# Optimization experiments

Hardware: AMD Instinct MI355X
Metric: run time of the kernel (lower is better)

## Reference

```python
import jax, jax.numpy as jnp
import numpy as np

D_MODEL = 1024
N_HEADS = 16
HEAD_DIM = D_MODEL // N_HEADS
WINDOW = 256


def setup_inputs() -> dict:
    key = jax.random.key(0)
    ks = jax.random.split(key, 5)
    s = 1.0 / np.sqrt(D_MODEL)
    x = jax.random.normal(ks[0], (1, 4096, D_MODEL), dtype=jnp.float32)
    W_qkv = jax.random.uniform(ks[1], (D_MODEL, 3 * D_MODEL), jnp.float32, -s, s)
    b_qkv = jax.random.uniform(ks[2], (3 * D_MODEL,), jnp.float32, -s, s)
    W_proj = jax.random.uniform(ks[3], (D_MODEL, D_MODEL), jnp.float32, -s, s)
    b_proj = jax.random.uniform(ks[4], (D_MODEL,), jnp.float32, -s, s)
    return {"x": x, "W_qkv": W_qkv, "b_qkv": b_qkv, "W_proj": W_proj, "b_proj": b_proj}


def reference(x, W_qkv, b_qkv, W_proj, b_proj):
    b, t, c = x.shape
    qkv = x @ W_qkv + b_qkv  # [b,t,3c]
    q, k, v = jnp.split(qkv, 3, axis=-1)
    # [b,h,t,d]
    q = q.reshape(b, t, N_HEADS, HEAD_DIM).transpose(0, 2, 1, 3)
    k = k.reshape(b, t, N_HEADS, HEAD_DIM).transpose(0, 2, 1, 3)
    v = v.reshape(b, t, N_HEADS, HEAD_DIM).transpose(0, 2, 1, 3)
    att = jnp.einsum('bhqd,bhkd->bhqk', q, k) / np.sqrt(HEAD_DIM)
    idx = jnp.arange(t)
    diff = idx[:, None] - idx[None, :]  # query - key
    allowed = (diff >= 0) & (diff < WINDOW)  # causal & local window
    att = jnp.where(allowed[None, None], att, -jnp.inf)
    att = jax.nn.softmax(att, axis=-1)
    y = jnp.einsum('bhqk,bhkd->bhqd', att, v)
    y = y.transpose(0, 2, 1, 3).reshape(b, t, c)
    return y @ W_proj + b_proj
```

## Files before the change

kernel.cpp:

```cpp
#include <hip/hip_runtime.h>
#include <stdint.h>

#define TSEQ 4096
#define DMODEL 1024
#define N3 3072
#define NHEADS 16
#define HDIM 64
#define WINDOW 256

typedef __attribute__((ext_vector_type(8))) short short8;
typedef __attribute__((ext_vector_type(4))) float f32x4;

__device__ __forceinline__ unsigned short f2bf(float f) {
  unsigned u = __builtin_bit_cast(unsigned, f);
  return (unsigned short)((u + 0x7fffu + ((u >> 16) & 1u)) >> 16);
}

__device__ __forceinline__ unsigned cvtpk(float lo, float hi) {
  unsigned r;
  asm("v_cvt_pk_bf16_f32 %0, %1, %2" : "=v"(r) : "v"(lo), "v"(hi));
  return r;
}

__device__ __forceinline__ f32x4 mfma16(short8 a, short8 b, f32x4 c) {
  return __builtin_amdgcn_mfma_f32_16x16x32_bf16(a, b, c, 0, 0, 0);
}

__device__ __forceinline__ void g2lds16(const void* g, void* l) {
  __builtin_amdgcn_global_load_lds(
      (const __attribute__((address_space(1))) void*)(uintptr_t)g,
      (__attribute__((address_space(3))) void*)(uintptr_t)l,
      16, 0, 0);
}


__global__ __launch_bounds__(256) void prep(const float* __restrict__ x,
                                            const float* __restrict__ Wqkv,
                                            const float* __restrict__ Wproj,
                                            unsigned short* __restrict__ xb,
                                            unsigned short* __restrict__ oQkvT,
                                            unsigned short* __restrict__ oProjT) {
  __shared__ float tile[32][33];
  int b = blockIdx.x;
  int tid = threadIdx.x;
  if (b < 4096) {
    int i = (b * 256 + tid) * 4;
    float4 v = *(const float4*)(x + i);
    unsigned lo = cvtpk(v.x, v.y), hi = cvtpk(v.z, v.w);
    unsigned long long packed = (unsigned long long)lo | ((unsigned long long)hi << 32);
    *(unsigned long long*)(xb + i) = packed;
    return;
  }
  b -= 4096;
  int bx = b & 127, by = b >> 7;
  const float* in;
  unsigned short* out;
  int C;
  if (bx < 96) {
    in = Wqkv; out = oQkvT; C = N3;
  } else {
    bx -= 96; in = Wproj; out = oProjT; C = DMODEL;
  }
  const int R = DMODEL;
  int c0 = bx * 32;
  int r0 = by * 32;
  int tx = tid & 31, ty = tid >> 5;
#pragma unroll
  for (int i = 0; i < 32; i += 8)
    tile[ty + i][tx] = in[(size_t)(r0 + ty + i) * C + c0 + tx];
  __syncthreads();
#pragma unroll
  for (int i = 0; i < 32; i += 8)
    out[(size_t)(c0 + ty + i) * R + r0 + tx] = f2bf(tile[tx][ty + i]);
}


template <int EPI, int MI, int NI>
__global__ __launch_bounds__(256)
void gemm_bf16(const unsigned short* __restrict__ A,
               const unsigned short* __restrict__ BT,
               const float* __restrict__ bias,
               unsigned short* __restrict__ oQ,
               unsigned short* __restrict__ oK,
               unsigned short* __restrict__ oVT,
               float* __restrict__ oF) {
  constexpr int BM = MI * 32, BN = NI * 32;
  constexpr int LPS = MI / 2 + NI / 2;
  __shared__ unsigned short Asm[2][BM * 32];
  __shared__ unsigned short Bsm[2][BN * 32];
  const int K = 1024;
  int m0 = blockIdx.x * BM;
  int n0 = blockIdx.y * BN;
  int tid = threadIdx.x;
  int w = tid >> 6, lane = tid & 63;
  int l15 = lane & 15, l4 = lane >> 4;
  int wm = (w >> 1) * (MI * 16), wn = (w & 1) * (NI * 16);

  f32x4 acc[MI][NI];
#pragma unroll
  for (int i = 0; i < MI; i++)
#pragma unroll
    for (int j = 0; j < NI; j++) acc[i][j] = (f32x4){0.f, 0.f, 0.f, 0.f};

  int lr = lane >> 2;
  int slot = ((lane & 3) * 16) ^ (((lr >> 1) & 3) << 4);
  const char* aG = (const char*)(A + (size_t)(m0 + w * (BM / 4) + lr) * K) + slot;
  const char* bG = (const char*)(BT + (size_t)(n0 + w * (BN / 4) + lr) * K) + slot;
  const size_t rowSkip = (size_t)16 * K * 2;

  auto stage = [&](int s, int b) {
    int koff = s * 64;
#pragma unroll
    for (int j = 0; j < MI / 2; j++)
      g2lds16(aG + j * rowSkip + koff, &Asm[b][(w * (MI / 2) + j) * 512]);
#pragma unroll
    for (int j = 0; j < NI / 2; j++)
      g2lds16(bG + j * rowSkip + koff, &Bsm[b][(w * (NI / 2) + j) * 512]);
  };

  int sX = ((l15 >> 1) & 3) << 4;

  auto compute = [&](int b) {
    short8 af[MI], bfr[NI];
#pragma unroll
    for (int mi = 0; mi < MI; mi++) {
      int rA = wm + mi * 16 + l15;
      af[mi] = *(const short8*)((const char*)Asm[b] + rA * 64 + ((l4 * 16) ^ sX));
    }
#pragma unroll
    for (int ni = 0; ni < NI; ni++) {
      int rB = wn + ni * 16 + l15;
      bfr[ni] = *(const short8*)((const char*)Bsm[b] + rB * 64 + ((l4 * 16) ^ sX));
    }
#pragma unroll
    for (int mi = 0; mi < MI; mi++)
#pragma unroll
      for (int ni = 0; ni < NI; ni++)
        acc[mi][ni] = mfma16(af[mi], bfr[ni], acc[mi][ni]);
  };

  const int NS = K / 32;
  stage(0, 0);
#pragma unroll 1
  for (int s = 0; s < NS; s++) {
    if (s + 1 < NS) {
      stage(s + 1, (s + 1) & 1);
      if constexpr (LPS == 3) asm volatile("s_waitcnt vmcnt(3)" ::: "memory");
      else if constexpr (LPS == 2) asm volatile("s_waitcnt vmcnt(2)" ::: "memory");
      else asm volatile("s_waitcnt vmcnt(4)" ::: "memory");
    } else {
      asm volatile("s_waitcnt vmcnt(0)" ::: "memory");
    }
    __builtin_amdgcn_s_barrier();
    __builtin_amdgcn_sched_barrier(0);
    compute(s & 1);
    __builtin_amdgcn_sched_barrier(0);
    __builtin_amdgcn_s_barrier();
  }

#pragma unroll
  for (int ni = 0; ni < NI; ni++) {
    int nn = n0 + wn + ni * 16 + l15;
    float bv = bias[nn];
    int c = nn & 1023;
    int hh = c >> 6, dd = c & 63;
#pragma unroll
    for (int mi = 0; mi < MI; mi++) {
      int mm = m0 + wm + mi * 16 + l4 * 4;
      float v0 = acc[mi][ni][0] + bv;
      float v1 = acc[mi][ni][1] + bv;
      float v2 = acc[mi][ni][2] + bv;
      float v3 = acc[mi][ni][3] + bv;
      if (EPI == 1) {
        oF[(size_t)(mm + 0) * 1024 + nn] = v0;
        oF[(size_t)(mm + 1) * 1024 + nn] = v1;
        oF[(size_t)(mm + 2) * 1024 + nn] = v2;
        oF[(size_t)(mm + 3) * 1024 + nn] = v3;
      } else if (nn < 1024) {
        oQ[((size_t)hh * TSEQ + mm + 0) * 64 + dd] = f2bf(v0 * 0.125f);
        oQ[((size_t)hh * TSEQ + mm + 1) * 64 + dd] = f2bf(v1 * 0.125f);
        oQ[((size_t)hh * TSEQ + mm + 2) * 64 + dd] = f2bf(v2 * 0.125f);
        oQ[((size_t)hh * TSEQ + mm + 3) * 64 + dd] = f2bf(v3 * 0.125f);
      } else if (nn < 2048) {
        oK[((size_t)hh * TSEQ + mm + 0) * 64 + dd] = f2bf(v0);
        oK[((size_t)hh * TSEQ + mm + 1) * 64 + dd] = f2bf(v1);
        oK[((size_t)hh * TSEQ + mm + 2) * 64 + dd] = f2bf(v2);
        oK[((size_t)hh * TSEQ + mm + 3) * 64 + dd] = f2bf(v3);
      } else {
        unsigned lo = cvtpk(v0, v1), hi = cvtpk(v2, v3);
        unsigned long long pv = (unsigned long long)lo | ((unsigned long long)hi << 32);
        *(unsigned long long*)(oVT + ((size_t)hh * 64 + dd) * TSEQ + mm) = pv;
      }
    }
  }
}


__global__ __launch_bounds__(256)
void attn_swa(const unsigned short* __restrict__ Qa,
              const unsigned short* __restrict__ Ka,
              const unsigned short* __restrict__ Vt,
              unsigned short* __restrict__ Y) {
  __shared__ __align__(16) char KV[2][16384];
  __shared__ __align__(16) unsigned char Pl[4][2048];
  int flat = blockIdx.x;
  int swz = (flat & 7) * 128 + (flat >> 3);
  int h = swz >> 6, qb = swz & 63;
  int w = threadIdx.x >> 6, lane = threadIdx.x & 63;
  int l15 = lane & 15, l4 = lane >> 4;
  int qrow0 = qb * 64 + w * 16;
  int q = qrow0 + l15;

  const unsigned short* qp = Qa + ((size_t)h * TSEQ + q) * 64 + l4 * 8;
  short8 qf0 = *(const short8*)qp;
  short8 qf1 = *(const short8*)(qp + 32);

  const char* kgb = (const char*)(Ka + (size_t)h * TSEQ * 64);
  const char* vgb = (const char*)(Vt + (size_t)h * 64 * TSEQ);

  auto stage = [&](int kt, int b) {
    int kbase = kt * 64;
    int sub = lane >> 3, slot = (lane & 7) * 16;
    if (w < 2) {
      int R0 = w * 32;
      const char* src = kgb + (size_t)kbase * 128;
#pragma unroll
      for (int j = 0; j < 4; j++) {
        int r = R0 + j * 8 + sub;
        g2lds16(src + r * 128 + (slot ^ ((r & 7) << 4)), &KV[b][R0 * 128 + j * 1024]);
      }
    } else {
      int D0 = (w - 2) * 32;
      const char* src = vgb + (size_t)kbase * 2;
#pragma unroll
      for (int j = 0; j < 4; j++) {
        int d = D0 + j * 8 + sub;
        g2lds16(src + (size_t)d * 8192 + (slot ^ ((d & 7) << 4)),
                &KV[b][8192 + D0 * 128 + j * 1024]);
      }
    }
  };

  float m = -1e30f, lsum = 0.f;
  f32x4 o[4];
#pragma unroll
  for (int ni = 0; ni < 4; ni++) o[ni] = (f32x4){0.f, 0.f, 0.f, 0.f};

  unsigned char* pw = Pl[w];
  int xw = (l15 & 7) << 4;

  auto compute = [&](int kt, int b, int MODE) {
    int kbase = kt * 64;
    const char* kb = KV[b];
    const char* vb = KV[b] + 8192;
    f32x4 s[4];
#pragma unroll
    for (int ni = 0; ni < 4; ni++) {
      int rb = (ni * 16 + l15) * 128;
      short8 k0 = *(const short8*)(kb + rb + ((l4 * 16) ^ xw));
      short8 k1 = *(const short8*)(kb + rb + ((64 + l4 * 16) ^ xw));
      f32x4 z = (f32x4){0.f, 0.f, 0.f, 0.f};
      z = mfma16(k0, qf0, z);
      s[ni] = mfma16(k1, qf1, z);
    }
    if (MODE != 0) {
#pragma unroll
      for (int ni = 0; ni < 4; ni++)
#pragma unroll
        for (int r = 0; r < 4; r++) {
          int key = kbase + ni * 16 + l4 * 4 + r;
          bool ok = (MODE == 2) ? (key <= q) : (q - key < WINDOW);
          s[ni][r] = ok ? s[ni][r] : -1e30f;
        }
    }
    float pm0 = fmaxf(fmaxf(s[0][0], s[0][1]), fmaxf(s[0][2], s[0][3]));
    float pm1 = fmaxf(fmaxf(s[1][0], s[1][1]), fmaxf(s[1][2], s[1][3]));
    float pm2 = fmaxf(fmaxf(s[2][0], s[2][1]), fmaxf(s[2][2], s[2][3]));
    float pm3 = fmaxf(fmaxf(s[3][0], s[3][1]), fmaxf(s[3][2], s[3][3]));
    float pm = fmaxf(fmaxf(pm0, pm1), fmaxf(pm2, pm3));
    pm = fmaxf(pm, __shfl_xor(pm, 16, 64));
    pm = fmaxf(pm, __shfl_xor(pm, 32, 64));
    float mn = fmaxf(m, pm);
    float alpha = __expf(m - mn);
    m = mn;
    float rs = 0.f;
#pragma unroll
    for (int ni = 0; ni < 4; ni++)
#pragma unroll
      for (int r = 0; r < 4; r++) {
        float p = __expf(s[ni][r] - mn);
        s[ni][r] = p;
        rs += p;
      }
    rs += __shfl_xor(rs, 16, 64);
    rs += __shfl_xor(rs, 32, 64);
    lsum = lsum * alpha + rs;
#pragma unroll
    for (int ni = 0; ni < 4; ni++) {
      unsigned lo = cvtpk(s[ni][0], s[ni][1]);
      unsigned hi = cvtpk(s[ni][2], s[ni][3]);
      unsigned long long pv = (unsigned long long)lo | ((unsigned long long)hi << 32);
      *(unsigned long long*)(pw + l15 * 128 + ((ni * 32 + l4 * 8) ^ xw)) = pv;
    }
    short8 pa0 = *(const short8*)(pw + l15 * 128 + ((l4 * 16) ^ xw));
    short8 pa1 = *(const short8*)(pw + l15 * 128 + ((64 + l4 * 16) ^ xw));
#pragma unroll
    for (int ni = 0; ni < 4; ni++)
#pragma unroll
      for (int r = 0; r < 4; r++) o[ni][r] *= alpha;
#pragma unroll
    for (int ni = 0; ni < 4; ni++) {
      int rb = (ni * 16 + l15) * 128;
      short8 v0 = *(const short8*)(vb + rb + ((l4 * 16) ^ xw));
      short8 v1 = *(const short8*)(vb + rb + ((64 + l4 * 16) ^ xw));
      o[ni] = mfma16(v0, pa0, o[ni]);
      o[ni] = mfma16(v1, pa1, o[ni]);
    }
  };

  int kt0 = qb >= 4 ? qb - 4 : 0;
  int NT = qb - kt0 + 1;
  stage(kt0, 0);
  for (int t = 0; t < NT; t++) {
    int kt = kt0 + t;
    if (t + 1 < NT) {
      stage(kt + 1, (t + 1) & 1);
      asm volatile("s_waitcnt vmcnt(4)" ::: "memory");
    } else {
      asm volatile("s_waitcnt vmcnt(0)" ::: "memory");
    }
    __builtin_amdgcn_s_barrier();
    __builtin_amdgcn_sched_barrier(0);
    int MODE = (t == NT - 1) ? 2 : ((qb >= 4 && t == 0) ? 1 : 0);
    compute(kt, t & 1, MODE);
    __builtin_amdgcn_sched_barrier(0);
    __builtin_amdgcn_s_barrier();
  }

  float inv = 1.f / lsum;
#pragma unroll
  for (int ni = 0; ni < 4; ni++) {
    unsigned lo = cvtpk(o[ni][0] * inv, o[ni][1] * inv);
    unsigned hi = cvtpk(o[ni][2] * inv, o[ni][3] * inv);
    unsigned long long yv = (unsigned long long)lo | ((unsigned long long)hi << 32);
    *(unsigned long long*)(Y + (size_t)q * DMODEL + h * 64 + ni * 16 + l4 * 4) = yv;
  }
}


extern "C" void kernel_launch(void* const* d_in, const int* in_sizes, int n_in,
                              void* d_out, int out_size, void* d_ws, size_t ws_size,
                              hipStream_t stream) {
  const float* x = (const float*)d_in[0];
  const float* Wqkv = (const float*)d_in[1];
  const float* bqkv = (const float*)d_in[2];
  const float* Wproj = (const float*)d_in[3];
  const float* bproj = (const float*)d_in[4];
  float* out = (float*)d_out;

  unsigned short* ws = (unsigned short*)d_ws;
  unsigned short* xb = ws;
  unsigned short* wqkvT = xb + (size_t)TSEQ * DMODEL;
  unsigned short* wprojT = wqkvT + (size_t)N3 * DMODEL;
  unsigned short* qarr = wprojT + (size_t)DMODEL * DMODEL;
  unsigned short* karr = qarr + (size_t)NHEADS * TSEQ * HDIM;
  unsigned short* vtarr = karr + (size_t)NHEADS * TSEQ * HDIM;
  unsigned short* yarr = vtarr + (size_t)NHEADS * TSEQ * HDIM;

  prep<<<8192, 256, 0, stream>>>(x, Wqkv, Wproj, xb, wqkvT, wprojT);
  gemm_bf16<0, 4, 2><<<dim3(TSEQ / 128, N3 / 64), 256, 0, stream>>>(xb, wqkvT, bqkv, qarr, karr, vtarr, nullptr);
  attn_swa<<<1024, 256, 0, stream>>>(qarr, karr, vtarr, yarr);
  gemm_bf16<1, 2, 2><<<dim3(TSEQ / 64, DMODEL / 64), 256, 0, stream>>>(yarr, wprojT, bproj, nullptr, nullptr, nullptr, out);
}
```

Before: 93.00 us.

## Share K/V tiles across two query blocks per attention workgroup and enlarge QKV GEMM tile

New measurement: 83.82 us (median of 2 runs). 9.9% less time.

```diff
diff --git a/kernel.cpp b/kernel.cpp
--- a/kernel.cpp
+++ b/kernel.cpp
@@ -104,18 +104,17 @@
 
   int lr = lane >> 2;
   int slot = ((lane & 3) * 16) ^ (((lr >> 1) & 3) << 4);
-  const char* aG = (const char*)(A + (size_t)(m0 + w * (BM / 4) + lr) * K) + slot;
-  const char* bG = (const char*)(BT + (size_t)(n0 + w * (BN / 4) + lr) * K) + slot;
-  const size_t rowSkip = (size_t)16 * K * 2;
+  const char* aG = (const char*)(A + (size_t)(m0 + w * (MI * 8) + lr) * K) + slot;
+  const char* bG = (const char*)(BT + (size_t)(n0 + w * (NI * 8) + lr) * K) + slot;
 
   auto stage = [&](int s, int b) {
     int koff = s * 64;
 #pragma unroll
-    for (int j = 0; j < MI / 2; j++)
-      g2lds16(aG + j * rowSkip + koff, &Asm[b][(w * (MI / 2) + j) * 512]);
+    for (int c = 0; c < MI / 2; c++)
+      g2lds16(aG + (size_t)c * 16 * 2048 + koff, &Asm[b][(w * (MI / 2) + c) * 512]);
 #pragma unroll
     for (int j = 0; j < NI / 2; j++)
-      g2lds16(bG + j * rowSkip + koff, &Bsm[b][(w * (NI / 2) + j) * 512]);
+      g2lds16(bG + (size_t)j * 16 * 2048 + koff, &Bsm[b][(w * (NI / 2) + j) * 512]);
   };
 
   int sX = ((l15 >> 1) & 3) << 4;
@@ -145,9 +144,8 @@
   for (int s = 0; s < NS; s++) {
     if (s + 1 < NS) {
       stage(s + 1, (s + 1) & 1);
-      if constexpr (LPS == 3) asm volatile("s_waitcnt vmcnt(3)" ::: "memory");
-      else if constexpr (LPS == 2) asm volatile("s_waitcnt vmcnt(2)" ::: "memory");
-      else asm volatile("s_waitcnt vmcnt(4)" ::: "memory");
+      if constexpr (LPS == 4) asm volatile("s_waitcnt vmcnt(4)" ::: "memory");
+      else asm volatile("s_waitcnt vmcnt(2)" ::: "memory");
     } else {
       asm volatile("s_waitcnt vmcnt(0)" ::: "memory");
     }
@@ -196,19 +194,21 @@
 }
 
 
-__global__ __launch_bounds__(256)
+__global__ __launch_bounds__(512)
 void attn_swa(const unsigned short* __restrict__ Qa,
               const unsigned short* __restrict__ Ka,
               const unsigned short* __restrict__ Vt,
               unsigned short* __restrict__ Y) {
   __shared__ __align__(16) char KV[2][16384];
-  __shared__ __align__(16) unsigned char Pl[4][2048];
+  __shared__ __align__(16) unsigned char Pl[8][2048];
   int flat = blockIdx.x;
-  int swz = (flat & 7) * 128 + (flat >> 3);
-  int h = swz >> 6, qb = swz & 63;
+  int swz = (flat & 7) * 64 + (flat >> 3);
+  int h = swz >> 5, qb2 = swz & 31;
   int w = threadIdx.x >> 6, lane = threadIdx.x & 63;
   int l15 = lane & 15, l4 = lane >> 4;
-  int qrow0 = qb * 64 + w * 16;
+  int g = w >> 2, wv = w & 3;
+  int qb = qb2 * 2 + g;
+  int qrow0 = qb * 64 + wv * 16;
   int q = qrow0 + l15;
 
   const unsigned short* qp = Qa + ((size_t)h * TSEQ + q) * 64 + l4 * 8;
@@ -218,27 +218,13 @@
   const char* kgb = (const char*)(Ka + (size_t)h * TSEQ * 64);
   const char* vgb = (const char*)(Vt + (size_t)h * 64 * TSEQ);
 
+  int sub8 = lane >> 3, slot = (lane & 7) * 16;
+  int r8 = w * 8 + sub8;
   auto stage = [&](int kt, int b) {
     int kbase = kt * 64;
-    int sub = lane >> 3, slot = (lane & 7) * 16;
-    if (w < 2) {
-      int R0 = w * 32;
-      const char* src = kgb + (size_t)kbase * 128;
-#pragma unroll
-      for (int j = 0; j < 4; j++) {
-        int r = R0 + j * 8 + sub;
-        g2lds16(src + r * 128 + (slot ^ ((r & 7) << 4)), &KV[b][R0 * 128 + j * 1024]);
-      }
-    } else {
-      int D0 = (w - 2) * 32;
-      const char* src = vgb + (size_t)kbase * 2;
-#pragma unroll
-      for (int j = 0; j < 4; j++) {
-        int d = D0 + j * 8 + sub;
-        g2lds16(src + (size_t)d * 8192 + (slot ^ ((d & 7) << 4)),
-                &KV[b][8192 + D0 * 128 + j * 1024]);
-      }
-    }
+    g2lds16(kgb + (size_t)(kbase + r8) * 128 + (slot ^ (sub8 << 4)), &KV[b][w * 1024]);
+    g2lds16(vgb + (size_t)r8 * 8192 + (size_t)kbase * 2 + (slot ^ (sub8 << 4)),
+            &KV[b][8192 + w * 1024]);
   };
 
   float m = -1e30f, lsum = 0.f;
@@ -254,6 +240,7 @@
     const char* kb = KV[b];
     const char* vb = KV[b] + 8192;
     f32x4 s[4];
+    __builtin_amdgcn_s_setprio(1);
 #pragma unroll
     for (int ni = 0; ni < 4; ni++) {
       int rb = (ni * 16 + l15) * 128;
@@ -263,6 +250,7 @@
       z = mfma16(k0, qf0, z);
       s[ni] = mfma16(k1, qf1, z);
     }
+    __builtin_amdgcn_s_setprio(0);
     if (MODE != 0) {
 #pragma unroll
       for (int ni = 0; ni < 4; ni++)
@@ -280,21 +268,28 @@
     float pm = fmaxf(fmaxf(pm0, pm1), fmaxf(pm2, pm3));
     pm = fmaxf(pm, __shfl_xor(pm, 16, 64));
     pm = fmaxf(pm, __shfl_xor(pm, 32, 64));
-    float mn = fmaxf(m, pm);
-    float alpha = __expf(m - mn);
-    m = mn;
+    if (!__all(pm <= m)) {
+      float mn = fmaxf(m, pm);
+      float alpha = __expf(m - mn);
+      m = mn;
+      lsum *= alpha;
+#pragma unroll
+      for (int ni = 0; ni < 4; ni++)
+#pragma unroll
+        for (int r = 0; r < 4; r++) o[ni][r] *= alpha;
+    }
     float rs = 0.f;
 #pragma unroll
     for (int ni = 0; ni < 4; ni++)
 #pragma unroll
       for (int r = 0; r < 4; r++) {
-        float p = __expf(s[ni][r] - mn);
+        float p = __expf(s[ni][r] - m);
         s[ni][r] = p;
         rs += p;
       }
     rs += __shfl_xor(rs, 16, 64);
     rs += __shfl_xor(rs, 32, 64);
-    lsum = lsum * alpha + rs;
+    lsum += rs;
 #pragma unroll
     for (int ni = 0; ni < 4; ni++) {
       unsigned lo = cvtpk(s[ni][0], s[ni][1]);
@@ -304,10 +299,7 @@
     }
     short8 pa0 = *(const short8*)(pw + l15 * 128 + ((l4 * 16) ^ xw));
     short8 pa1 = *(const short8*)(pw + l15 * 128 + ((64 + l4 * 16) ^ xw));
-#pragma unroll
-    for (int ni = 0; ni < 4; ni++)
-#pragma unroll
-      for (int r = 0; r < 4; r++) o[ni][r] *= alpha;
+    __builtin_amdgcn_s_setprio(1);
 #pragma unroll
     for (int ni = 0; ni < 4; ni++) {
       int rb = (ni * 16 + l15) * 128;
@@ -316,23 +308,28 @@
       o[ni] = mfma16(v0, pa0, o[ni]);
       o[ni] = mfma16(v1, pa1, o[ni]);
     }
+    __builtin_amdgcn_s_setprio(0);
   };
 
-  int kt0 = qb >= 4 ? qb - 4 : 0;
-  int NT = qb - kt0 + 1;
-  stage(kt0, 0);
+  int qbA = qb2 * 2, qbB = qbA + 1;
+  int ktLo = qbA >= 4 ? qbA - 4 : 0;
+  int NT = qbB - ktLo + 1;
+  stage(ktLo, 0);
   for (int t = 0; t < NT; t++) {
-    int kt = kt0 + t;
+    int kt = ktLo + t;
     if (t + 1 < NT) {
       stage(kt + 1, (t + 1) & 1);
-      asm volatile("s_waitcnt vmcnt(4)" ::: "memory");
+      asm volatile("s_waitcnt vmcnt(2)" ::: "memory");
     } else {
       asm volatile("s_waitcnt vmcnt(0)" ::: "memory");
     }
     __builtin_amdgcn_s_barrier();
     __builtin_amdgcn_sched_barrier(0);
-    int MODE = (t == NT - 1) ? 2 : ((qb >= 4 && t == 0) ? 1 : 0);
-    compute(kt, t & 1, MODE);
+    bool active = (g == 0) ? (kt <= qbA) : (kt >= qbB - 4);
+    if (active) {
+      int MODE = (kt == qb) ? 2 : ((qb >= 4 && kt == qb - 4) ? 1 : 0);
+      compute(kt, t & 1, MODE);
+    }
     __builtin_amdgcn_sched_barrier(0);
     __builtin_amdgcn_s_barrier();
   }
@@ -368,7 +365,9 @@
   unsigned short* yarr = vtarr + (size_t)NHEADS * TSEQ * HDIM;
 
   prep<<<8192, 256, 0, stream>>>(x, Wqkv, Wproj, xb, wqkvT, wprojT);
-  gemm_bf16<0, 4, 2><<<dim3(TSEQ / 128, N3 / 64), 256, 0, stream>>>(xb, wqkvT, bqkv, qarr, karr, vtarr, nullptr);
-  attn_swa<<<1024, 256, 0, stream>>>(qarr, karr, vtarr, yarr);
-  gemm_bf16<1, 2, 2><<<dim3(TSEQ / 64, DMODEL / 64), 256, 0, stream>>>(yarr, wprojT, bproj, nullptr, nullptr, nullptr, out);
-}
+  gemm_bf16<0, 4, 4><<<dim3(TSEQ / 128, N3 / 128), 256, 0, stream>>>(
+      xb, wqkvT, bqkv, qarr, karr, vtarr, nullptr);
+  attn_swa<<<512, 512, 0, stream>>>(qarr, karr, vtarr, yarr);
+  gemm_bf16<1, 2, 2><<<dim3(TSEQ / 64, DMODEL / 64), 256, 0, stream>>>(
+      yarr, wprojT, bproj, nullptr, nullptr, nullptr, out);
+}
```
